# Optimization experiments

Hardware: AMD Instinct MI355X
Metric: run time of the kernel (lower is better)

The kernel has to match this reference:

```python
import jax, jax.numpy as jnp
import numpy as np

H = 1024  # hidden_size == input_size
L = 2     # num_layers


def _gru_cell(x, h, W_ih, W_hh, b_ih, b_hh):
    # PyTorch GRUCell math. x:[B,D], h:[B,H]
    gi = x @ W_ih.T + b_ih          # [B,3H]
    gh = h @ W_hh.T + b_hh          # [B,3H]
    i_r, i_z, i_n = jnp.split(gi, 3, axis=-1)
    h_r, h_z, h_n = jnp.split(gh, 3, axis=-1)
    r = jax.nn.sigmoid(i_r + h_r)
    z = jax.nn.sigmoid(i_z + h_z)
    n = jnp.tanh(i_n + r * h_n)
    return (1.0 - z) * n + z * h


def setup_inputs() -> dict:
    key = jax.random.key(0)
    ks = jax.random.split(key, 16)
    B, T = 64, 256
    s = 0.05
    x = jax.random.normal(ks[0], (B, T, H), dtype=jnp.float32)
    h0 = jnp.zeros((1, H), dtype=jnp.float32)
    lengths = jnp.maximum(jax.random.randint(ks[1], (B,), 0, T + 1), 1).astype(jnp.int32)
    W_ih = jax.random.normal(ks[2], (L, 3 * H, H), dtype=jnp.float32) * s
    W_hh = jax.random.normal(ks[3], (L, 3 * H, H), dtype=jnp.float32) * s
    b_ih = jax.random.normal(ks[4], (L, 3 * H), dtype=jnp.float32) * s
    b_hh = jax.random.normal(ks[5], (L, 3 * H), dtype=jnp.float32) * s
    gW1 = jax.random.normal(ks[6], (H, H), dtype=jnp.float32) * s
    gb1 = jax.random.normal(ks[7], (H,), dtype=jnp.float32) * s
    gW2 = jax.random.normal(ks[8], (H, H), dtype=jnp.float32) * s
    gb2 = jax.random.normal(ks[9], (H,), dtype=jnp.float32) * s
    gWF = jax.random.normal(ks[10], (1, H), dtype=jnp.float32) * s
    gbF = jax.random.normal(ks[11], (1,), dtype=jnp.float32) * s
    return {"x": x, "h0": h0, "input_lengths": lengths,
            "W_ih": W_ih, "W_hh": W_hh, "b_ih": b_ih, "b_hh": b_hh,
            "gW1": gW1, "gb1": gb1, "gW2": gW2, "gb2": gb2,
            "gWF": gWF, "gbF": gbF}


def reference(x, h0, input_lengths, W_ih, W_hh, b_ih, b_hh, gW1, gb1, gW2, gb2, gWF, gbF):
    B, T, _ = x.shape
    h0b = jnp.broadcast_to(h0, (B, H))                      # [B,H]
    init_h = jnp.broadcast_to(h0b[None], (L, B, H))         # [L,B,H]
    x_t = jnp.swapaxes(x, 0, 1)                             # [T,B,D]
    x_next = jnp.concatenate([x_t[1:], x_t[-1:]], axis=0)   # x[t+1], last repeated (unused)
    ts = jnp.arange(T, dtype=jnp.int32)

    def step(ht, inp):
        xt, xnext, t = inp
        cur = xt
        new_h = []
        for n in range(L):  # dropout is identity at inference
            hn = _gru_cell(cur, ht[n], W_ih[n], W_hh[n], b_ih[n], b_hh[n])
            new_h.append(hn)
            cur = hn
        ht_new = jnp.stack(new_h)                           # [L,B,H]
        out_t = cur                                         # [B,H]
        # BinaryGate(x_{t+1}, ht_n)
        y = xnext @ gW1.T + gb1 + out_t @ gW2.T + gb2       # [B,H]
        g_raw = jax.nn.sigmoid(y @ gWF.T + gbF)[:, 0]       # [B]
        is_last = t == (input_lengths - 1)
        gt = jnp.where(is_last, 1.0, g_raw)
        valid = t < input_lengths
        out_m = jnp.where(valid[:, None], out_t, 0.0)
        gt_m = jnp.where(valid, gt, 0.0)
        reset = (gt > 0.5) & valid
        ht_next = jnp.where(reset[None, :, None], h0b[None], ht_new)
        ht_next = jnp.where(valid[None, :, None], ht_next, ht)
        return ht_next, (out_m, gt_m)

    _, (outs, gates) = jax.lax.scan(step, init_h, (x_t, x_next, ts))
    output = jnp.swapaxes(outs, 0, 1)                       # [B,T,H]
    gate_z = jnp.swapaxes(gates, 0, 1)                      # [B,T]
    return output, gate_z
```

## Files before the change

### kernel.cpp

```cpp
#include <hip/hip_runtime.h>
#include <cmath>

#define Bsz 64
#define Tsz 256
#define Hsz 1024
#define NWG 256
#define NTHR 512
#define GRPWG 64
#define WROW 522

#define WAITVM(N) do {                                            \
    asm volatile("s_waitcnt vmcnt(" #N ")" ::: "memory");         \
    __builtin_amdgcn_sched_barrier(0);                            \
} while (0)

__device__ float g_h[2][2][Bsz * Hsz];
__device__ float g_pre[2][Bsz];
__device__ float g_an[Tsz * Bsz];
__device__ float g_v1[Hsz];
__device__ float g_v2[Hsz];
__device__ float g_c;
__device__ unsigned g_bar_cnt[4 * 32];
__device__ unsigned g_bar_gen[4 * 32];
__device__ float g_gi0[(size_t)Tsz * Bsz * 3 * Hsz];

__device__ __forceinline__ float ldc(const float* p) {
    return __hip_atomic_load((const float*)p, __ATOMIC_RELAXED,
                             __HIP_MEMORY_SCOPE_AGENT);
}
__device__ __forceinline__ void stc(float* p, float v) {
    __hip_atomic_store(p, v, __ATOMIC_RELAXED, __HIP_MEMORY_SCOPE_AGENT);
}

__device__ __forceinline__ void ldc4_issue(const float* p, float4& v) {
    asm volatile("global_load_dwordx4 %0, %1, off sc0 sc1"
                 : "=v"(v) : "v"(p));
}

__device__ __forceinline__ float4 bfx4(uint2 u) {
    float4 f;
    f.x = __uint_as_float(u.x << 16);
    f.y = __uint_as_float(u.x & 0xffff0000u);
    f.z = __uint_as_float(u.y << 16);
    f.w = __uint_as_float(u.y & 0xffff0000u);
    return f;
}

__device__ __forceinline__ unsigned rne_bf16_pair(float a, float b) {
    unsigned u0 = __float_as_uint(a);
    unsigned u1 = __float_as_uint(b);
    u0 = (u0 + 0x7fffu + ((u0 >> 16) & 1u)) >> 16;
    u1 = (u1 + 0x7fffu + ((u1 >> 16) & 1u)) >> 16;
    return u0 | (u1 << 16);
}

__device__ __forceinline__ void groupbar(int bg, unsigned lgen) {
    __syncthreads();
    if (threadIdx.x == 0) {
        unsigned* cnt = &g_bar_cnt[bg * 32];
        unsigned* gen = &g_bar_gen[bg * 32];
        unsigned prev = __hip_atomic_fetch_add(cnt, 1u, __ATOMIC_RELAXED,
                                               __HIP_MEMORY_SCOPE_AGENT);
        if (prev == lgen * GRPWG - 1u) {
            __hip_atomic_store(gen, lgen, __ATOMIC_RELAXED,
                               __HIP_MEMORY_SCOPE_AGENT);
        } else {
            while (__hip_atomic_load(gen, __ATOMIC_RELAXED,
                                     __HIP_MEMORY_SCOPE_AGENT) < lgen)
                __builtin_amdgcn_s_sleep(1);
        }
    }
    __syncthreads();
}

__global__ void k_init(const float* __restrict__ h0,
                       const float* __restrict__ gW1, const float* __restrict__ gb1,
                       const float* __restrict__ gW2, const float* __restrict__ gb2,
                       const float* __restrict__ gWF, const float* __restrict__ gbF) {
    int blk = blockIdx.x, tid = threadIdx.x;
    if (blk < 256) {
        int idx = blk * 256 + tid;
        float v = h0[idx & (Hsz - 1)];
        g_h[0][0][idx] = v;
        g_h[1][0][idx] = v;
    } else if (blk == 256) {
        __shared__ float red[256];
        float s = 0.f;
        for (int j = tid; j < Hsz; j += 256) s += gWF[j] * (gb1[j] + gb2[j]);
        red[tid] = s;
        __syncthreads();
        for (int off = 128; off > 0; off >>= 1) {
            if (tid < off) red[tid] += red[tid + off];
            __syncthreads();
        }
        if (tid == 0) g_c = red[0] + gbF[0];
        if (tid < 128) ((float*)g_pre)[tid] = 0.f;
        if (tid >= 128 && tid < 256) {
            g_bar_cnt[tid - 128] = 0u;
            g_bar_gen[tid - 128] = 0u;
        }
    } else if (blk < 261) {
        int k = (blk - 257) * 256 + tid;
        float s = 0.f;
        for (int j = 0; j < Hsz; ++j) s += gWF[j] * gW1[(size_t)j * Hsz + k];
        g_v1[k] = s;
    } else {
        int k = (blk - 261) * 256 + tid;
        float s = 0.f;
        for (int j = 0; j < Hsz; ++j) s += gWF[j] * gW2[(size_t)j * Hsz + k];
        g_v2[k] = s;
    }
}

__global__ void k_an(const float* __restrict__ x) {
    int blk = blockIdx.x, tid = threadIdx.x;
    int lane = tid & 63, wv = tid >> 6;
    for (int i = 0; i < 16; ++i) {
        int o = blk * 64 + wv * 16 + i;
        int b = o >> 8, tt = o & 255;
        int ts = (tt + 1 < Tsz) ? tt + 1 : Tsz - 1;
        const float* xp = x + ((size_t)b * Tsz + ts) * Hsz;
        float s = 0.f;
        for (int k = lane; k < Hsz; k += 64) s += xp[k] * g_v1[k];
        for (int m = 32; m > 0; m >>= 1) s += __shfl_xor(s, m, 64);
        if (lane == 0) g_an[tt * 64 + b] = s;
    }
}

__global__ __launch_bounds__(256) void k_gemm(const float* __restrict__ x,
                                              const float* __restrict__ Wih,
                                              const float* __restrict__ bih) {
    __shared__ float As[16][132];
    __shared__ float Bs[16][132];
    const int tid = threadIdx.x;
    const int n0 = blockIdx.x * 128;
    const int m0 = blockIdx.y * 128;
    const int tx = tid & 15, ty = tid >> 4;
    float acc[8][8] = {};

    for (int k0 = 0; k0 < Hsz; k0 += 16) {
#pragma unroll
        for (int i = 0; i < 2; ++i) {
            int task = tid * 2 + i;
            int rl = task >> 2;
            int kq = task & 3;
            int r = m0 + rl;
            int bb = r & 63, tt = r >> 6;
            float4 v = *(const float4*)(x + ((size_t)bb * Tsz + tt) * Hsz + k0 + kq * 4);
            As[kq * 4 + 0][rl] = v.x; As[kq * 4 + 1][rl] = v.y;
            As[kq * 4 + 2][rl] = v.z; As[kq * 4 + 3][rl] = v.w;
            float4 w = *(const float4*)(Wih + (size_t)(n0 + rl) * Hsz + k0 + kq * 4);
            Bs[kq * 4 + 0][rl] = w.x; Bs[kq * 4 + 1][rl] = w.y;
            Bs[kq * 4 + 2][rl] = w.z; Bs[kq * 4 + 3][rl] = w.w;
        }
        __syncthreads();
#pragma unroll
        for (int k = 0; k < 16; ++k) {
            float a[8], b[8];
            *(float4*)&a[0] = *(float4*)&As[k][ty * 8];
            *(float4*)&a[4] = *(float4*)&As[k][ty * 8 + 4];
            *(float4*)&b[0] = *(float4*)&Bs[k][tx * 8];
            *(float4*)&b[4] = *(float4*)&Bs[k][tx * 8 + 4];
#pragma unroll
            for (int i2 = 0; i2 < 8; ++i2)
#pragma unroll
                for (int j2 = 0; j2 < 8; ++j2) acc[i2][j2] += a[i2] * b[j2];
        }
        __syncthreads();
    }
#pragma unroll
    for (int i2 = 0; i2 < 8; ++i2) {
        int r = m0 + ty * 8 + i2;
        float* cp = g_gi0 + (size_t)r * (3 * Hsz) + n0 + tx * 8;
#pragma unroll
        for (int j2 = 0; j2 < 8; j2 += 4) {
            float4 v;
            v.x = acc[i2][j2 + 0] + bih[n0 + tx * 8 + j2 + 0];
            v.y = acc[i2][j2 + 1] + bih[n0 + tx * 8 + j2 + 1];
            v.z = acc[i2][j2 + 2] + bih[n0 + tx * 8 + j2 + 2];
            v.w = acc[i2][j2 + 3] + bih[n0 + tx * 8 + j2 + 3];
            *(float4*)(cp + j2) = v;
        }
    }
}

__device__ __forceinline__ float dot4(float4 a, float4 b) {
    return a.x * b.x + a.y * b.y + a.z * b.z + a.w * b.w;
}

__device__ __forceinline__ void phaseA(
    int t, int b0, int jn0,
    const float* __restrict__ st0, float* __restrict__ ho0,
    const float* __restrict__ st1,
    const float* __restrict__ Whh1,
    const float* __restrict__ bh0,
    const float* __restrict__ h0,
    const unsigned* s_wl,
    float (*s_act)[2][16][36], float (*s_red)[4][16][16],
    const float* __restrict__ s_rst,
    float (&axh)[3][2][2]) {

    const int tid = threadIdx.x;
    const int wv = tid >> 6, lane = tid & 63;
    const int bi2 = (lane & 7) * 2, ji2 = (lane >> 3) * 2;
    const int kq0 = wv * 128;

    int rb[6];
    const float* wp1[6];
#pragma unroll
    for (int g = 0; g < 3; ++g)
#pragma unroll
        for (int dj = 0; dj < 2; ++dj) {
            rb[g * 2 + dj] = (g * 16 + ji2 + dj) * WROW;
            wp1[g * 2 + dj] = Whh1 + (size_t)(g * Hsz + jn0 + ji2 + dj) * Hsz;
        }

    float acc0[3][2][2] = {};
#pragma unroll
    for (int m = 0; m < 3; ++m)
#pragma unroll
        for (int a = 0; a < 2; ++a)
#pragma unroll
            for (int d = 0; d < 2; ++d) axh[m][a][d] = 0.f;

    auto issue_chunk = [&](int c, float4* dst) {
        const int kb = kq0 + c * 32;
#pragma unroll
        for (int i = 0; i < 4; ++i) {
            int o = (i & 1) * 64 + lane;
            int layer = i >> 1;
            int bb = (o >> 3) & 15, k4 = o & 7;
            int k = kb + k4 * 4;
            const float* p = (layer ? st1 : st0) + (size_t)(b0 + bb) * Hsz + k;
            ldc4_issue(p, dst[i]);
        }
    };
    auto patch_write = [&](int c, float4* src) {
        const int kb = kq0 + c * 32;
#pragma unroll
        for (int i = 0; i < 4; ++i) {
            int o = (i & 1) * 64 + lane;
            int layer = i >> 1;
            int bb = (o >> 3) & 15, k4 = o & 7;
            int k = kb + k4 * 4;
            float4 v = src[i];
            float4 hv = *(const float4*)(h0 + k);
            if (s_rst[bb] != 0.f) v = hv;
            *(float4*)&s_act[wv][layer][bb][k4 * 4] = v;
        }
    };
    auto compute_chunk = [&](int c) {
        const int kb = kq0 + c * 32;
#pragma unroll 2
        for (int kk = 0; kk < 32; kk += 4) {
            const int k = kb + kk;
            const int kw = k >> 1;
            float4 hA = *(const float4*)&s_act[wv][0][bi2][kk];
            float4 hB = *(const float4*)&s_act[wv][0][bi2 + 1][kk];
            float4 gA = *(const float4*)&s_act[wv][1][bi2][kk];
            float4 gB = *(const float4*)&s_act[wv][1][bi2 + 1][kk];
#pragma unroll
            for (int dj = 0; dj < 2; ++dj) {
                float4 whr = bfx4(*(const uint2*)&s_wl[rb[0 * 2 + dj] + kw]);
                float4 whz = bfx4(*(const uint2*)&s_wl[rb[1 * 2 + dj] + kw]);
                float4 whn = bfx4(*(const uint2*)&s_wl[rb[2 * 2 + dj] + kw]);
                acc0[0][0][dj] += dot4(hA, whr);
                acc0[0][1][dj] += dot4(hB, whr);
                acc0[1][0][dj] += dot4(hA, whz);
                acc0[1][1][dj] += dot4(hB, whz);
                acc0[2][0][dj] += dot4(hA, whn);
                acc0[2][1][dj] += dot4(hB, whn);
                float4 w1r = *(const float4*)(wp1[0 * 2 + dj] + k);
                float4 w1z = *(const float4*)(wp1[1 * 2 + dj] + k);
                float4 w1n = *(const float4*)(wp1[2 * 2 + dj] + k);
                axh[0][0][dj] += dot4(gA, w1r);
                axh[0][1][dj] += dot4(gB, w1r);
                axh[1][0][dj] += dot4(gA, w1z);
                axh[1][1][dj] += dot4(gB, w1z);
                axh[2][0][dj] += dot4(gA, w1n);
                axh[2][1][dj] += dot4(gB, w1n);
            }
        }
    };

    float4 C0[4], C1[4], C2[4], C3[4];
    issue_chunk(0, C0); issue_chunk(1, C1);
    issue_chunk(2, C2); issue_chunk(3, C3);
    WAITVM(12);
    patch_write(0, C0); compute_chunk(0);
    WAITVM(8);
    patch_write(1, C1); compute_chunk(1);
    WAITVM(4);
    patch_write(2, C2); compute_chunk(2);
    WAITVM(0);
    patch_write(3, C3); compute_chunk(3);

    __syncthreads();
    if (wv >= 4) {
#pragma unroll
        for (int m = 0; m < 3; ++m)
#pragma unroll
            for (int db = 0; db < 2; ++db)
#pragma unroll
                for (int dj = 0; dj < 2; ++dj)
                    s_red[wv - 4][m][bi2 + db][ji2 + dj] = acc0[m][db][dj];
    }
    __syncthreads();
    if (wv < 4) {
#pragma unroll
        for (int m = 0; m < 3; ++m)
#pragma unroll
            for (int db = 0; db < 2; ++db)
#pragma unroll
                for (int dj = 0; dj < 2; ++dj)
                    s_red[wv][m][bi2 + db][ji2 + dj] += acc0[m][db][dj];
    }
    __syncthreads();

    if (tid < 256) {
        const int ji = tid & 15, bI = tid >> 4;
        const int b = b0 + bI, jn = jn0 + ji;
        float hprev = ldc(st0 + (size_t)b * Hsz + jn);
        const float* gp = g_gi0 + (size_t)(t * 64 + b) * (3 * Hsz) + jn;
        float g0r = gp[0];
        float g0z = gp[Hsz];
        float g0n = gp[2 * Hsz];
        float s[3];
#pragma unroll
        for (int m = 0; m < 3; ++m)
            s[m] = s_red[0][m][bI][ji] + s_red[1][m][bI][ji] +
                   s_red[2][m][bI][ji] + s_red[3][m][bI][ji];
        if (s_rst[bI] != 0.f) hprev = h0[jn];

        const float pr  = g0r + s[0] + bh0[jn];
        const float pz  = g0z + s[1] + bh0[Hsz + jn];
        const float pin = g0n;
        const float phn = s[2] + bh0[2 * Hsz + jn];
        const float r_ = 1.f / (1.f + __expf(-pr));
        const float z_ = 1.f / (1.f + __expf(-pz));
        const float n_ = tanhf(pin + r_ * phn);
        const float hnew = (1.f - z_) * n_ + z_ * hprev;
        stc(ho0 + (size_t)b * Hsz + jn, hnew);
    }
}

__device__ __forceinline__ void phaseB(
    int t, int b0, int jn0,
    const float* __restrict__ a0,
    const float* __restrict__ st, float* __restrict__ ho,
    const float* __restrict__ Wih1,
    const float* __restrict__ bi, const float* __restrict__ bh,
    const float* __restrict__ h0, const int* __restrict__ lens,
    float* __restrict__ outp,
    float (*s_act)[2][16][36], float (*s_red)[4][16][16],
    const float* __restrict__ s_rst, float (*s_gs)[16],
    const float (&axh)[3][2][2]) {

    const int tid = threadIdx.x;
    const int wv = tid >> 6, lane = tid & 63;
    const int bi2 = (lane & 7) * 2, ji2 = (lane >> 3) * 2;
    const int kq0 = wv * 128;

    const float* wpi[6];
#pragma unroll
    for (int g = 0; g < 3; ++g)
#pragma unroll
        for (int dj = 0; dj < 2; ++dj)
            wpi[g * 2 + dj] = Wih1 + (size_t)(g * Hsz + jn0 + ji2 + dj) * Hsz;

    float acc[3][2][2] = {};

    auto issue_chunk = [&](int c, float4* dst) {
        const int kb = kq0 + c * 32;
#pragma unroll
        for (int i = 0; i < 2; ++i) {
            int o = i * 64 + lane;
            int bb = (o >> 3) & 15, k4 = o & 7;
            int k = kb + k4 * 4;
            ldc4_issue(a0 + (size_t)(b0 + bb) * Hsz + k, dst[i]);
        }
    };
    auto write_chunk = [&](int c, float4* src) {
#pragma unroll
        for (int i = 0; i < 2; ++i) {
            int o = i * 64 + lane;
            int bb = (o >> 3) & 15, k4 = o & 7;
            *(float4*)&s_act[wv][0][bb][k4 * 4] = src[i];
        }
    };
    auto compute_chunk = [&](int c) {
        const int kb = kq0 + c * 32;
#pragma unroll 2
        for (int kk = 0; kk < 32; kk += 4) {
            const int k = kb + kk;
            float4 xA = *(const float4*)&s_act[wv][0][bi2][kk];
            float4 xB = *(const float4*)&s_act[wv][0][bi2 + 1][kk];
#pragma unroll
            for (int dj = 0; dj < 2; ++dj) {
                float4 wir = *(const float4*)(wpi[0 * 2 + dj] + k);
                float4 wiz = *(const float4*)(wpi[1 * 2 + dj] + k);
                float4 win = *(const float4*)(wpi[2 * 2 + dj] + k);
                acc[0][0][dj] += dot4(xA, wir);
                acc[0][1][dj] += dot4(xB, wir);
                acc[1][0][dj] += dot4(xA, wiz);
                acc[1][1][dj] += dot4(xB, wiz);
                acc[2][0][dj] += dot4(xA, win);
                acc[2][1][dj] += dot4(xB, win);
            }
        }
    };

    float4 C0[2], C1[2], C2[2], C3[2];
    issue_chunk(0, C0); issue_chunk(1, C1);
    issue_chunk(2, C2); issue_chunk(3, C3);
    WAITVM(6);
    write_chunk(0, C0); compute_chunk(0);
    WAITVM(4);
    write_chunk(1, C1); compute_chunk(1);
    WAITVM(2);
    write_chunk(2, C2); compute_chunk(2);
    WAITVM(0);
    write_chunk(3, C3); compute_chunk(3);

    float m4[4][2][2];
#pragma unroll
    for (int db = 0; db < 2; ++db)
#pragma unroll
        for (int dj = 0; dj < 2; ++dj) {
            m4[0][db][dj] = acc[0][db][dj] + axh[0][db][dj];
            m4[1][db][dj] = acc[1][db][dj] + axh[1][db][dj];
            m4[2][db][dj] = acc[2][db][dj];
            m4[3][db][dj] = axh[2][db][dj];
        }

    __syncthreads();
    if (wv >= 4) {
#pragma unroll
        for (int m = 0; m < 4; ++m)
#pragma unroll
            for (int db = 0; db < 2; ++db)
#pragma unroll
                for (int dj = 0; dj < 2; ++dj)
                    s_red[wv - 4][m][bi2 + db][ji2 + dj] = m4[m][db][dj];
    }
    __syncthreads();
    if (wv < 4) {
#pragma unroll
        for (int m = 0; m < 4; ++m)
#pragma unroll
            for (int db = 0; db < 2; ++db)
#pragma unroll
                for (int dj = 0; dj < 2; ++dj)
                    s_red[wv][m][bi2 + db][ji2 + dj] += m4[m][db][dj];
    }
    __syncthreads();

    if (tid < 256) {
        const int ji = tid & 15, bI = tid >> 4;
        const int b = b0 + bI, jn = jn0 + ji;
        float hprev = ldc(st + (size_t)b * Hsz + jn);
        const int lb = lens[b];
        float s[4];
#pragma unroll
        for (int m = 0; m < 4; ++m)
            s[m] = s_red[0][m][bI][ji] + s_red[1][m][bI][ji] +
                   s_red[2][m][bI][ji] + s_red[3][m][bI][ji];
        if (s_rst[bI] != 0.f) hprev = h0[jn];

        const float pr  = s[0] + bi[jn] + bh[jn];
        const float pz  = s[1] + bi[Hsz + jn] + bh[Hsz + jn];
        const float pin = s[2] + bi[2 * Hsz + jn];
        const float phn = s[3] + bh[2 * Hsz + jn];
        const float r_ = 1.f / (1.f + __expf(-pr));
        const float z_ = 1.f / (1.f + __expf(-pz));
        const float n_ = tanhf(pin + r_ * phn);
        const float hnew = (1.f - z_) * n_ + z_ * hprev;
        stc(ho + (size_t)b * Hsz + jn, hnew);
        outp[((size_t)b * Tsz + t) * Hsz + jn] = (t < lb) ? hnew : 0.f;
        s_gs[bI][ji] = hnew * g_v2[jn];
    }
    __syncthreads();
    if (tid < 16) {
        float sm = 0.f;
#pragma unroll
        for (int j = 0; j < 16; ++j) sm += s_gs[tid][j];
        atomicAdd(&g_pre[t & 1][b0 + tid], sm);
    }
}

__global__ void __launch_bounds__(NTHR, 1)
k_main(const float* __restrict__ h0, const int* __restrict__ lens,
       const float* __restrict__ W_ih, const float* __restrict__ W_hh,
       const float* __restrict__ b_ih, const float* __restrict__ b_hh,
       float* __restrict__ outp, float* __restrict__ gatep) {
    __shared__ __align__(16) unsigned s_w[48 * WROW];
    __shared__ __align__(16) float s_act[8][2][16][36];
    __shared__ float s_red[4][4][16][16];
    __shared__ float s_rst[16];
    __shared__ float s_gs[16][16];

    const int tid = threadIdx.x;
    const int wg = blockIdx.x, bg = wg >> 6, jg = wg & 63;
    const int b0 = bg * 16, jn0 = jg * 16;
    unsigned lgen = 0;

    const float* Wih1 = W_ih + (size_t)3 * Hsz * Hsz;
    const float* Whh1 = W_hh + (size_t)3 * Hsz * Hsz;
    const float* bi1 = b_ih + 3 * Hsz;
    const float* bh1 = b_hh + 3 * Hsz;

    for (int idx = tid; idx < 48 * 512; idx += NTHR) {
        int r = idx >> 9, kw = idx & 511;
        int g = r >> 4, j = r & 15;
        const float* wrow = W_hh + ((size_t)(g * Hsz + jn0 + j)) * Hsz + kw * 2;
        s_w[r * WROW + kw] = rne_bf16_pair(wrow[0], wrow[1]);
    }
    __syncthreads();

    float axh[3][2][2];

    for (int t = 0; t < Tsz; ++t) {
        const int p0 = t & 1, p1 = p0 ^ 1;

        if (tid < 16) {
            float rstf = 0.f;
            const int b = b0 + tid;
            const int lb = lens[b];
            if (t > 0) {
                const int tp = t - 1;
                const float pre = g_c + g_an[tp * 64 + b] + ldc(&g_pre[p1][b]);
                const bool il = (tp == lb - 1);
                rstf = (il || pre > 0.f) ? 1.f : 0.f;
                if (jg == 0) {
                    const float gt = il ? 1.f : 1.f / (1.f + __expf(-pre));
                    gatep[(size_t)b * Tsz + tp] = (tp < lb) ? gt : 0.f;
                }
            }
            s_rst[tid] = rstf;
        }
        __syncthreads();

        phaseA(t, b0, jn0,
               g_h[0][p0], g_h[0][p1], g_h[1][p0],
               Whh1, b_hh, h0, s_w, s_act, s_red, s_rst, axh);
        groupbar(bg, ++lgen);

        if (jg == 0 && tid < 16) stc(&g_pre[p1][b0 + tid], 0.f);

        phaseB(t, b0, jn0,
               g_h[0][p1], g_h[1][p0], g_h[1][p1],
               Wih1, bi1, bh1, h0, lens,
               outp, s_act, s_red, s_rst, s_gs, axh);
        groupbar(bg, ++lgen);
    }

    if (jg == 0 && tid < 16) {
        const int b = b0 + tid;
        const int lb = lens[b];
        const int tp = Tsz - 1;
        const float pre = g_c + g_an[tp * 64 + b] + ldc(&g_pre[tp & 1][b]);
        const bool il = (tp == lb - 1);
        const float gt = il ? 1.f : 1.f / (1.f + __expf(-pre));
        gatep[(size_t)b * Tsz + tp] = (tp < lb) ? gt : 0.f;
    }
}

extern "C" void kernel_launch(void* const* d_in, const int* in_sizes, int n_in,
                              void* d_out, int out_size, void* d_ws, size_t ws_size,
                              hipStream_t stream) {
    const float* x = (const float*)d_in[0];
    const float* h0 = (const float*)d_in[1];
    const int* lens = (const int*)d_in[2];
    const float* W_ih = (const float*)d_in[3];
    const float* W_hh = (const float*)d_in[4];
    const float* b_ih = (const float*)d_in[5];
    const float* b_hh = (const float*)d_in[6];
    const float* gW1 = (const float*)d_in[7];
    const float* gb1 = (const float*)d_in[8];
    const float* gW2 = (const float*)d_in[9];
    const float* gb2 = (const float*)d_in[10];
    const float* gWF = (const float*)d_in[11];
    const float* gbF = (const float*)d_in[12];
    float* outp = (float*)d_out;
    float* gatep = outp + (size_t)Bsz * Tsz * Hsz;

    hipLaunchKernelGGL(k_init, dim3(265), dim3(256), 0, stream,
                       h0, gW1, gb1, gW2, gb2, gWF, gbF);
    hipLaunchKernelGGL(k_an, dim3(256), dim3(256), 0, stream, x);
    hipLaunchKernelGGL(k_gemm, dim3(24, 128), dim3(256), 0, stream,
                       x, W_ih, b_ih);

    void* args[8] = { (void*)&h0, (void*)&lens, (void*)&W_ih, (void*)&W_hh,
                      (void*)&b_ih, (void*)&b_hh, (void*)&outp, (void*)&gatep };
    hipError_t err = hipLaunchCooperativeKernel((const void*)k_main, dim3(NWG), dim3(NTHR),
                                                args, 0, stream);
    (void)err;
}
```

Measured before the change: 13.00 ms.

## Move bf16 W_hh0 to global and double workgroups with narrower column slices

Layer-0 recurrent weights are pre-packed to bf16 in a global buffer by a new kernel, so they are no longer held in per-workgroup LDS. That frees shared memory, and each workgroup now handles 8 hidden columns instead of 16. With two workgroups per CU, 512 workgroups are launched; otherwise each workgroup loops over two column slices. The gain is more parallelism and occupancy, at the cost of reading the weights from global/L2 each step and synchronising 128 workgroups per barrier group.

```diff
diff --git a/kernel.cpp b/kernel.cpp
--- a/kernel.cpp
+++ b/kernel.cpp
@@ -4,10 +4,8 @@
 #define Bsz 64
 #define Tsz 256
 #define Hsz 1024
-#define NWG 256
 #define NTHR 512
-#define GRPWG 64
-#define WROW 522
+#define WROWU 512
 
 #define WAITVM(N) do {                                            \
     asm volatile("s_waitcnt vmcnt(" #N ")" ::: "memory");         \
@@ -23,6 +21,7 @@
 __device__ unsigned g_bar_cnt[4 * 32];
 __device__ unsigned g_bar_gen[4 * 32];
 __device__ float g_gi0[(size_t)Tsz * Bsz * 3 * Hsz];
+__device__ unsigned g_w0[(size_t)3 * Hsz * WROWU];
 
 __device__ __forceinline__ float ldc(const float* p) {
     return __hip_atomic_load((const float*)p, __ATOMIC_RELAXED,
@@ -54,14 +53,14 @@
     return u0 | (u1 << 16);
 }
 
-__device__ __forceinline__ void groupbar(int bg, unsigned lgen) {
+__device__ __forceinline__ void groupbar(int bg, unsigned lgen, unsigned grp) {
     __syncthreads();
     if (threadIdx.x == 0) {
         unsigned* cnt = &g_bar_cnt[bg * 32];
         unsigned* gen = &g_bar_gen[bg * 32];
         unsigned prev = __hip_atomic_fetch_add(cnt, 1u, __ATOMIC_RELAXED,
                                                __HIP_MEMORY_SCOPE_AGENT);
-        if (prev == lgen * GRPWG - 1u) {
+        if (prev == lgen * grp - 1u) {
             __hip_atomic_store(gen, lgen, __ATOMIC_RELAXED,
                                __HIP_MEMORY_SCOPE_AGENT);
         } else {
@@ -112,6 +111,14 @@
     }
 }
 
+__global__ __launch_bounds__(256) void k_pack0(const float* __restrict__ W_hh) {
+    const int r = blockIdx.x;
+    const float* src = W_hh + (size_t)r * Hsz;
+    unsigned* dst = g_w0 + (size_t)r * WROWU;
+    for (int i = threadIdx.x; i < WROWU; i += 256)
+        dst[i] = rne_bf16_pair(src[2 * i], src[2 * i + 1]);
+}
+
 __global__ void k_an(const float* __restrict__ x) {
     int blk = blockIdx.x, tid = threadIdx.x;
     int lane = tid & 63, wv = tid >> 6;
@@ -192,36 +199,31 @@
     int t, int b0, int jn0,
     const float* __restrict__ st0, float* __restrict__ ho0,
     const float* __restrict__ st1,
-    const float* __restrict__ Whh1,
-    const float* __restrict__ bh0,
+    const float* __restrict__ Whh1, const float* __restrict__ bh0,
     const float* __restrict__ h0,
-    const unsigned* s_wl,
-    float (*s_act)[2][16][36], float (*s_red)[4][16][16],
+    float (*s_act)[2][16][36], float (*s_red)[4][16][8],
     const float* __restrict__ s_rst,
-    float (&axh)[3][2][2]) {
+    float (&axh)[3][2]) {
 
     const int tid = threadIdx.x;
     const int wv = tid >> 6, lane = tid & 63;
-    const int bi2 = (lane & 7) * 2, ji2 = (lane >> 3) * 2;
+    const int bi2 = (lane & 7) * 2, ji = lane >> 3;
     const int kq0 = wv * 128;
 
-    int rb[6];
-    const float* wp1[6];
-#pragma unroll
-    for (int g = 0; g < 3; ++g)
-#pragma unroll
-        for (int dj = 0; dj < 2; ++dj) {
-            rb[g * 2 + dj] = (g * 16 + ji2 + dj) * WROW;
-            wp1[g * 2 + dj] = Whh1 + (size_t)(g * Hsz + jn0 + ji2 + dj) * Hsz;
-        }
-
-    float acc0[3][2][2] = {};
+    const unsigned* w0p[3];
+    const float* w1p[3];
+#pragma unroll
+    for (int g = 0; g < 3; ++g) {
+        int row = g * Hsz + jn0 + ji;
+        w0p[g] = g_w0 + (size_t)row * WROWU;
+        w1p[g] = Whh1 + (size_t)row * Hsz;
+    }
+
+    float acc0[3][2] = {};
 #pragma unroll
     for (int m = 0; m < 3; ++m)
 #pragma unroll
-        for (int a = 0; a < 2; ++a)
-#pragma unroll
-            for (int d = 0; d < 2; ++d) axh[m][a][d] = 0.f;
+        for (int d = 0; d < 2; ++d) axh[m][d] = 0.f;
 
     auto issue_chunk = [&](int c, float4* dst) {
         const int kb = kq0 + c * 32;
@@ -259,27 +261,24 @@
             float4 hB = *(const float4*)&s_act[wv][0][bi2 + 1][kk];
             float4 gA = *(const float4*)&s_act[wv][1][bi2][kk];
             float4 gB = *(const float4*)&s_act[wv][1][bi2 + 1][kk];
-#pragma unroll
-            for (int dj = 0; dj < 2; ++dj) {
-                float4 whr = bfx4(*(const uint2*)&s_wl[rb[0 * 2 + dj] + kw]);
-                float4 whz = bfx4(*(const uint2*)&s_wl[rb[1 * 2 + dj] + kw]);
-                float4 whn = bfx4(*(const uint2*)&s_wl[rb[2 * 2 + dj] + kw]);
-                acc0[0][0][dj] += dot4(hA, whr);
-                acc0[0][1][dj] += dot4(hB, whr);
-                acc0[1][0][dj] += dot4(hA, whz);
-                acc0[1][1][dj] += dot4(hB, whz);
-                acc0[2][0][dj] += dot4(hA, whn);
-                acc0[2][1][dj] += dot4(hB, whn);
-                float4 w1r = *(const float4*)(wp1[0 * 2 + dj] + k);
-                float4 w1z = *(const float4*)(wp1[1 * 2 + dj] + k);
-                float4 w1n = *(const float4*)(wp1[2 * 2 + dj] + k);
-                axh[0][0][dj] += dot4(gA, w1r);
-                axh[0][1][dj] += dot4(gB, w1r);
-                axh[1][0][dj] += dot4(gA, w1z);
-                axh[1][1][dj] += dot4(gB, w1z);
-                axh[2][0][dj] += dot4(gA, w1n);
-                axh[2][1][dj] += dot4(gB, w1n);
-            }
+            float4 whr = bfx4(*(const uint2*)(w0p[0] + kw));
+            float4 whz = bfx4(*(const uint2*)(w0p[1] + kw));
+            float4 whn = bfx4(*(const uint2*)(w0p[2] + kw));
+            acc0[0][0] += dot4(hA, whr);
+            acc0[0][1] += dot4(hB, whr);
+            acc0[1][0] += dot4(hA, whz);
+            acc0[1][1] += dot4(hB, whz);
+            acc0[2][0] += dot4(hA, whn);
+            acc0[2][1] += dot4(hB, whn);
+            float4 w1r = *(const float4*)(w1p[0] + k);
+            float4 w1z = *(const float4*)(w1p[1] + k);
+            float4 w1n = *(const float4*)(w1p[2] + k);
+            axh[0][0] += dot4(gA, w1r);
+            axh[0][1] += dot4(gB, w1r);
+            axh[1][0] += dot4(gA, w1z);
+            axh[1][1] += dot4(gB, w1z);
+            axh[2][0] += dot4(gA, w1n);
+            axh[2][1] += dot4(gB, w1n);
         }
     };
 
@@ -301,9 +300,7 @@
         for (int m = 0; m < 3; ++m)
 #pragma unroll
             for (int db = 0; db < 2; ++db)
-#pragma unroll
-                for (int dj = 0; dj < 2; ++dj)
-                    s_red[wv - 4][m][bi2 + db][ji2 + dj] = acc0[m][db][dj];
+                s_red[wv - 4][m][bi2 + db][ji] = acc0[m][db];
     }
     __syncthreads();
     if (wv < 4) {
@@ -311,15 +308,13 @@
         for (int m = 0; m < 3; ++m)
 #pragma unroll
             for (int db = 0; db < 2; ++db)
-#pragma unroll
-                for (int dj = 0; dj < 2; ++dj)
-                    s_red[wv][m][bi2 + db][ji2 + dj] += acc0[m][db][dj];
-    }
-    __syncthreads();
-
-    if (tid < 256) {
-        const int ji = tid & 15, bI = tid >> 4;
-        const int b = b0 + bI, jn = jn0 + ji;
+                s_red[wv][m][bi2 + db][ji] += acc0[m][db];
+    }
+    __syncthreads();
+
+    if (tid < 128) {
+        const int ji2 = tid & 7, bI = tid >> 3;
+        const int b = b0 + bI, jn = jn0 + ji2;
         float hprev = ldc(st0 + (size_t)b * Hsz + jn);
         const float* gp = g_gi0 + (size_t)(t * 64 + b) * (3 * Hsz) + jn;
         float g0r = gp[0];
@@ -328,8 +323,8 @@
         float s[3];
 #pragma unroll
         for (int m = 0; m < 3; ++m)
-            s[m] = s_red[0][m][bI][ji] + s_red[1][m][bI][ji] +
-                   s_red[2][m][bI][ji] + s_red[3][m][bI][ji];
+            s[m] = s_red[0][m][bI][ji2] + s_red[1][m][bI][ji2] +
+                   s_red[2][m][bI][ji2] + s_red[3][m][bI][ji2];
         if (s_rst[bI] != 0.f) hprev = h0[jn];
 
         const float pr  = g0r + s[0] + bh0[jn];
@@ -352,23 +347,21 @@
     const float* __restrict__ bi, const float* __restrict__ bh,
     const float* __restrict__ h0, const int* __restrict__ lens,
     float* __restrict__ outp,
-    float (*s_act)[2][16][36], float (*s_red)[4][16][16],
-    const float* __restrict__ s_rst, float (*s_gs)[16],
-    const float (&axh)[3][2][2]) {
+    float (*s_act)[2][16][36], float (*s_red)[4][16][8],
+    const float* __restrict__ s_rst, float (*s_gs)[8],
+    const float (&axh)[3][2]) {
 
     const int tid = threadIdx.x;
     const int wv = tid >> 6, lane = tid & 63;
-    const int bi2 = (lane & 7) * 2, ji2 = (lane >> 3) * 2;
+    const int bi2 = (lane & 7) * 2, ji = lane >> 3;
     const int kq0 = wv * 128;
 
-    const float* wpi[6];
+    const float* wpi[3];
 #pragma unroll
     for (int g = 0; g < 3; ++g)
-#pragma unroll
-        for (int dj = 0; dj < 2; ++dj)
-            wpi[g * 2 + dj] = Wih1 + (size_t)(g * Hsz + jn0 + ji2 + dj) * Hsz;
-
-    float acc[3][2][2] = {};
+        wpi[g] = Wih1 + (size_t)(g * Hsz + jn0 + ji) * Hsz;
+
+    float acc[3][2] = {};
 
     auto issue_chunk = [&](int c, float4* dst) {
         const int kb = kq0 + c * 32;
@@ -395,18 +388,15 @@
             const int k = kb + kk;
             float4 xA = *(const float4*)&s_act[wv][0][bi2][kk];
             float4 xB = *(const float4*)&s_act[wv][0][bi2 + 1][kk];
-#pragma unroll
-            for (int dj = 0; dj < 2; ++dj) {
-                float4 wir = *(const float4*)(wpi[0 * 2 + dj] + k);
-                float4 wiz = *(const float4*)(wpi[1 * 2 + dj] + k);
-                float4 win = *(const float4*)(wpi[2 * 2 + dj] + k);
-                acc[0][0][dj] += dot4(xA, wir);
-                acc[0][1][dj] += dot4(xB, wir);
-                acc[1][0][dj] += dot4(xA, wiz);
-                acc[1][1][dj] += dot4(xB, wiz);
-                acc[2][0][dj] += dot4(xA, win);
-                acc[2][1][dj] += dot4(xB, win);
-            }
+            float4 wir = *(const float4*)(wpi[0] + k);
+            float4 wiz = *(const float4*)(wpi[1] + k);
+            float4 win = *(const float4*)(wpi[2] + k);
+            acc[0][0] += dot4(xA, wir);
+            acc[0][1] += dot4(xB, wir);
+            acc[1][0] += dot4(xA, wiz);
+            acc[1][1] += dot4(xB, wiz);
+            acc[2][0] += dot4(xA, win);
+            acc[2][1] += dot4(xB, win);
         }
     };
 
@@ -422,16 +412,14 @@
     WAITVM(0);
     write_chunk(3, C3); compute_chunk(3);
 
-    float m4[4][2][2];
-#pragma unroll
-    for (int db = 0; db < 2; ++db)
-#pragma unroll
-        for (int dj = 0; dj < 2; ++dj) {
-            m4[0][db][dj] = acc[0][db][dj] + axh[0][db][dj];
-            m4[1][db][dj] = acc[1][db][dj] + axh[1][db][dj];
-            m4[2][db][dj] = acc[2][db][dj];
-            m4[3][db][dj] = axh[2][db][dj];
-        }
+    float m4[4][2];
+#pragma unroll
+    for (int db = 0; db < 2; ++db) {
+        m4[0][db] = acc[0][db] + axh[0][db];
+        m4[1][db] = acc[1][db] + axh[1][db];
+        m4[2][db] = acc[2][db];
+        m4[3][db] = axh[2][db];
+    }
 
     __syncthreads();
     if (wv >= 4) {
@@ -439,9 +427,7 @@
         for (int m = 0; m < 4; ++m)
 #pragma unroll
             for (int db = 0; db < 2; ++db)
-#pragma unroll
-                for (int dj = 0; dj < 2; ++dj)
-                    s_red[wv - 4][m][bi2 + db][ji2 + dj] = m4[m][db][dj];
+                s_red[wv - 4][m][bi2 + db][ji] = m4[m][db];
     }
     __syncthreads();
     if (wv < 4) {
@@ -449,22 +435,20 @@
         for (int m = 0; m < 4; ++m)
 #pragma unroll
             for (int db = 0; db < 2; ++db)
-#pragma unroll
-                for (int dj = 0; dj < 2; ++dj)
-                    s_red[wv][m][bi2 + db][ji2 + dj] += m4[m][db][dj];
-    }
-    __syncthreads();
-
-    if (tid < 256) {
-        const int ji = tid & 15, bI = tid >> 4;
-        const int b = b0 + bI, jn = jn0 + ji;
+                s_red[wv][m][bi2 + db][ji] += m4[m][db];
+    }
+    __syncthreads();
+
+    if (tid < 128) {
+        const int ji2 = tid & 7, bI = tid >> 3;
+        const int b = b0 + bI, jn = jn0 + ji2;
         float hprev = ldc(st + (size_t)b * Hsz + jn);
         const int lb = lens[b];
         float s[4];
 #pragma unroll
         for (int m = 0; m < 4; ++m)
-            s[m] = s_red[0][m][bI][ji] + s_red[1][m][bI][ji] +
-                   s_red[2][m][bI][ji] + s_red[3][m][bI][ji];
+            s[m] = s_red[0][m][bI][ji2] + s_red[1][m][bI][ji2] +
+                   s_red[2][m][bI][ji2] + s_red[3][m][bI][ji2];
         if (s_rst[bI] != 0.f) hprev = h0[jn];
 
         const float pr  = s[0] + bi[jn] + bh[jn];
@@ -477,31 +461,35 @@
         const float hnew = (1.f - z_) * n_ + z_ * hprev;
         stc(ho + (size_t)b * Hsz + jn, hnew);
         outp[((size_t)b * Tsz + t) * Hsz + jn] = (t < lb) ? hnew : 0.f;
-        s_gs[bI][ji] = hnew * g_v2[jn];
+        s_gs[bI][ji2] = hnew * g_v2[jn];
     }
     __syncthreads();
     if (tid < 16) {
         float sm = 0.f;
 #pragma unroll
-        for (int j = 0; j < 16; ++j) sm += s_gs[tid][j];
+        for (int j = 0; j < 8; ++j) sm += s_gs[tid][j];
         atomicAdd(&g_pre[t & 1][b0 + tid], sm);
     }
 }
 
+template <int JC>
 __global__ void __launch_bounds__(NTHR, 1)
 k_main(const float* __restrict__ h0, const int* __restrict__ lens,
        const float* __restrict__ W_ih, const float* __restrict__ W_hh,
        const float* __restrict__ b_ih, const float* __restrict__ b_hh,
        float* __restrict__ outp, float* __restrict__ gatep) {
-    __shared__ __align__(16) unsigned s_w[48 * WROW];
     __shared__ __align__(16) float s_act[8][2][16][36];
-    __shared__ float s_red[4][4][16][16];
+    __shared__ float s_red[4][4][16][8];
     __shared__ float s_rst[16];
-    __shared__ float s_gs[16][16];
+    __shared__ float s_gs[16][8];
+
+    constexpr int JSHIFT = (JC == 1) ? 7 : 6;
+    constexpr unsigned GRP = (JC == 1) ? 128u : 64u;
 
     const int tid = threadIdx.x;
-    const int wg = blockIdx.x, bg = wg >> 6, jg = wg & 63;
-    const int b0 = bg * 16, jn0 = jg * 16;
+    const int wg = blockIdx.x;
+    const int bg = wg >> JSHIFT, jbase = wg & (GRP - 1);
+    const int b0 = bg * 16;
     unsigned lgen = 0;
 
     const float* Wih1 = W_ih + (size_t)3 * Hsz * Hsz;
@@ -509,15 +497,7 @@
     const float* bi1 = b_ih + 3 * Hsz;
     const float* bh1 = b_hh + 3 * Hsz;
 
-    for (int idx = tid; idx < 48 * 512; idx += NTHR) {
-        int r = idx >> 9, kw = idx & 511;
-        int g = r >> 4, j = r & 15;
-        const float* wrow = W_hh + ((size_t)(g * Hsz + jn0 + j)) * Hsz + kw * 2;
-        s_w[r * WROW + kw] = rne_bf16_pair(wrow[0], wrow[1]);
-    }
-    __syncthreads();
-
-    float axh[3][2][2];
+    float axh[JC][3][2];
 
     for (int t = 0; t < Tsz; ++t) {
         const int p0 = t & 1, p1 = p0 ^ 1;
@@ -531,7 +511,7 @@
                 const float pre = g_c + g_an[tp * 64 + b] + ldc(&g_pre[p1][b]);
                 const bool il = (tp == lb - 1);
                 rstf = (il || pre > 0.f) ? 1.f : 0.f;
-                if (jg == 0) {
+                if (jbase == 0) {
                     const float gt = il ? 1.f : 1.f / (1.f + __expf(-pre));
                     gatep[(size_t)b * Tsz + tp] = (tp < lb) ? gt : 0.f;
                 }
@@ -540,21 +520,25 @@
         }
         __syncthreads();
 
-        phaseA(t, b0, jn0,
-               g_h[0][p0], g_h[0][p1], g_h[1][p0],
-               Whh1, b_hh, h0, s_w, s_act, s_red, s_rst, axh);
-        groupbar(bg, ++lgen);
-
-        if (jg == 0 && tid < 16) stc(&g_pre[p1][b0 + tid], 0.f);
-
-        phaseB(t, b0, jn0,
-               g_h[0][p1], g_h[1][p0], g_h[1][p1],
-               Wih1, bi1, bh1, h0, lens,
-               outp, s_act, s_red, s_rst, s_gs, axh);
-        groupbar(bg, ++lgen);
-    }
-
-    if (jg == 0 && tid < 16) {
+#pragma unroll
+        for (int j = 0; j < JC; ++j)
+            phaseA(t, b0, (jbase + j * (int)GRP) * 8,
+                   g_h[0][p0], g_h[0][p1], g_h[1][p0],
+                   Whh1, b_hh, h0, s_act, s_red, s_rst, axh[j]);
+        groupbar(bg, ++lgen, GRP);
+
+        if (jbase == 0 && tid < 16) stc(&g_pre[p1][b0 + tid], 0.f);
+
+#pragma unroll
+        for (int j = 0; j < JC; ++j)
+            phaseB(t, b0, (jbase + j * (int)GRP) * 8,
+                   g_h[0][p1], g_h[1][p0], g_h[1][p1],
+                   Wih1, bi1, bh1, h0, lens,
+                   outp, s_act, s_red, s_rst, s_gs, axh[j]);
+        groupbar(bg, ++lgen, GRP);
+    }
+
+    if (jbase == 0 && tid < 16) {
         const int b = b0 + tid;
         const int lb = lens[b];
         const int tp = Tsz - 1;
@@ -586,13 +570,28 @@
 
     hipLaunchKernelGGL(k_init, dim3(265), dim3(256), 0, stream,
                        h0, gW1, gb1, gW2, gb2, gWF, gbF);
+    hipLaunchKernelGGL(k_pack0, dim3(3072), dim3(256), 0, stream, W_hh);
     hipLaunchKernelGGL(k_an, dim3(256), dim3(256), 0, stream, x);
     hipLaunchKernelGGL(k_gemm, dim3(24, 128), dim3(256), 0, stream,
                        x, W_ih, b_ih);
 
+    static int s_mode = 0;
+    if (s_mode == 0) {
+        int mb = 0;
+        if (hipOccupancyMaxActiveBlocksPerMultiprocessor(
+                &mb, (const void*)k_main<1>, NTHR, 0) != hipSuccess) mb = 1;
+        s_mode = (mb >= 2) ? 1 : 2;
+    }
+
     void* args[8] = { (void*)&h0, (void*)&lens, (void*)&W_ih, (void*)&W_hh,
                       (void*)&b_ih, (void*)&b_hh, (void*)&outp, (void*)&gatep };
-    hipError_t err = hipLaunchCooperativeKernel((const void*)k_main, dim3(NWG), dim3(NTHR),
-                                                args, 0, stream);
+    hipError_t err;
+    if (s_mode == 1) {
+        err = hipLaunchCooperativeKernel((const void*)k_main<1>, dim3(512),
+                                         dim3(NTHR), args, 0, stream);
+    } else {
+        err = hipLaunchCooperativeKernel((const void*)k_main<2>, dim3(256),
+                                         dim3(NTHR), args, 0, stream);
+    }
     (void)err;
 }
```

Result: slower. 16.08 ms (+23.7%).
